# Kernel optimization log

Hardware: AMD Instinct MI355X
Metric: run time of the kernel (lower is better)

The kernel has to match this reference:

```python
import jax, jax.numpy as jnp
import numpy as np

B, L, C, H = 4, 2048, 1024, 16
D = C // H
MAX_SCALE_MUL = float(np.log(100.0))
EPS = 1e-12


def setup_inputs() -> dict:
    key = jax.random.key(0)
    ks = jax.random.split(key, 7)
    return {
        "x": jax.random.normal(ks[0], (B, L, C), dtype=jnp.float32),
        "W_qkv": jax.random.normal(ks[1], (3 * C, C), dtype=jnp.float32) * (C ** -0.5),
        "q_bias": jax.random.normal(ks[2], (C,), dtype=jnp.float32) * 0.02,
        "v_bias": jax.random.normal(ks[3], (C,), dtype=jnp.float32) * 0.02,
        "scale_mul_log": jnp.full((1, H, 1, 1), np.log(4.0), dtype=jnp.float32),
        "W_proj": jax.random.normal(ks[4], (C, C), dtype=jnp.float32) * (C ** -0.5),
        "b_proj": jax.random.normal(ks[5], (C,), dtype=jnp.float32) * 0.02,
    }


def reference(x, W_qkv, q_bias, v_bias, scale_mul_log, W_proj, b_proj):
    Bb, Ll, Cc = x.shape
    # fused QKV projection with bias = cat(q_bias, zeros, v_bias)
    bias = jnp.concatenate([q_bias, jnp.zeros_like(q_bias), v_bias])
    qkv = (x @ W_qkv.T + bias).reshape(Bb, Ll, 3, H, D)
    q, k, v = (jnp.transpose(qkv[:, :, i], (0, 2, 1, 3)) for i in range(3))  # [B,H,L,D]
    # L2-norm attention: normalize q,k; learned per-head scale on q (clamped)
    scale_mul = jnp.exp(jnp.minimum(scale_mul_log, MAX_SCALE_MUL))  # [1,H,1,1]
    q = q / jnp.maximum(jnp.linalg.norm(q, axis=-1, keepdims=True), EPS) * scale_mul
    k = k / jnp.maximum(jnp.linalg.norm(k, axis=-1, keepdims=True), EPS)
    # SDPA with scale=1 (attn_l2_norm path), no mask, no dropout (eval)
    scores = jnp.einsum("bhqd,bhkd->bhqk", q, k)
    attn = jax.nn.softmax(scores, axis=-1)
    out = jnp.einsum("bhqk,bhkd->bhqd", attn, v)
    out = jnp.transpose(out, (0, 2, 1, 3)).reshape(Bb, Ll, Cc)
    return out @ W_proj.T + b_proj
```

## Files before the change

kernel.cpp:

```cpp
#include <hip/hip_runtime.h>
#include <hip/hip_bf16.h>


typedef __attribute__((ext_vector_type(8))) short bf16x8;
typedef __attribute__((ext_vector_type(16))) float f32x16;

#define MAXLOG 4.60517018598809f
#define LOG2E  1.4426950408889634f

__device__ __forceinline__ float bf2f(unsigned short u) {
    union { unsigned int i; float f; } v; v.i = ((unsigned int)u) << 16; return v.f;
}
__device__ __forceinline__ unsigned short f2bf(float f) {
    union { float f; unsigned int i; } v; v.f = f;
    unsigned int x = v.i;
    return (unsigned short)((x + 0x7FFFu + ((x >> 16) & 1u)) >> 16);
}
__device__ __forceinline__ unsigned fbits(float f) {
    union { float f; unsigned u; } v; v.f = f; return v.u;
}
__device__ __forceinline__ bf16x8 pack8(const float* __restrict__ p) {
    float4 a = *(const float4*)p;
    float4 b = *(const float4*)(p + 4);
    bf16x8 r;
    r[0] = (short)f2bf(a.x); r[1] = (short)f2bf(a.y);
    r[2] = (short)f2bf(a.z); r[3] = (short)f2bf(a.w);
    r[4] = (short)f2bf(b.x); r[5] = (short)f2bf(b.y);
    r[6] = (short)f2bf(b.z); r[7] = (short)f2bf(b.w);
    return r;
}
__device__ __forceinline__ void gload_lds16(const void* g, void* l) {
    __builtin_amdgcn_global_load_lds((const __attribute__((address_space(1))) void*)g,
                                     (__attribute__((address_space(3))) void*)l, 16, 0, 0);
}

__global__ __launch_bounds__(256) void k_prep(
    const float* __restrict__ x, const float* __restrict__ Wqkv,
    const float* __restrict__ Wp, const float* __restrict__ qbia,
    const float* __restrict__ vbia,
    unsigned short* __restrict__ xb, unsigned short* __restrict__ Wqkvb,
    unsigned short* __restrict__ Wpb, float* __restrict__ bias3)
{
    int i = blockIdx.x * 256 + threadIdx.x;
    if (i < 1048576) {
        *(bf16x8*)&xb[(long)i * 8] = pack8(&x[(long)i * 8]);
    } else if (i < 1441792) {
        int j = i - 1048576;
        *(bf16x8*)&Wqkvb[(long)j * 8] = pack8(&Wqkv[(long)j * 8]);
    } else if (i < 1572864) {
        int j = i - 1441792;
        *(bf16x8*)&Wpb[(long)j * 8] = pack8(&Wp[(long)j * 8]);
    } else if (i < 1573248) {
        int j = (i - 1572864) * 8;
        for (int u = 0; u < 8; ++u) {
            int n = j + u;
            float v = 0.0f;
            if (n < 1024) v = qbia[n];
            else if (n >= 2048) v = vbia[n - 2048];
            bias3[n] = v;
        }
    }
}

template<bool OUT_F32>
__global__ __launch_bounds__(256) void k_gemm_lds(
    const unsigned short* __restrict__ A, const unsigned short* __restrict__ Bh,
    const float* __restrict__ bias, void* __restrict__ Cp, int N, int K)
{
    __shared__ unsigned short As[128 * 32];
    __shared__ unsigned short Bs[128 * 32];
    const int t = threadIdx.x, wave = t >> 6, lane = t & 63;
    const int m32 = lane & 31, half = lane >> 5;
    const int bm = blockIdx.x * 128, bn = blockIdx.y * 128;
    const int wr = (wave >> 1) * 64, wc = (wave & 1) * 64;
    f32x16 acc[2][2] = {};

    const int srow = lane >> 2;
    const int scol = (lane & 3) * 8;
    const int c0 = wave * 2, c1 = wave * 2 + 1;
    const long ga0 = (long)(bm + c0 * 16 + srow) * K + scol;
    const long ga1 = (long)(bm + c1 * 16 + srow) * K + scol;
    const long gb0 = (long)(bn + c0 * 16 + srow) * K + scol;
    const long gb1 = (long)(bn + c1 * 16 + srow) * K + scol;

    for (int kt = 0; kt < K; kt += 32) {
        __syncthreads();
        gload_lds16(&A[ga0 + kt], &As[c0 * 512]);
        gload_lds16(&A[ga1 + kt], &As[c1 * 512]);
        gload_lds16(&Bh[gb0 + kt], &Bs[c0 * 512]);
        gload_lds16(&Bh[gb1 + kt], &Bs[c1 * 512]);
        __syncthreads();
        bf16x8 af[2][2], bfr[2][2];
        for (int mt = 0; mt < 2; ++mt)
            for (int f = 0; f < 2; ++f)
                af[mt][f] = *(const bf16x8*)&As[(wr + mt * 32 + m32) * 32 + f * 16 + half * 8];
        for (int nt = 0; nt < 2; ++nt)
            for (int f = 0; f < 2; ++f)
                bfr[nt][f] = *(const bf16x8*)&Bs[(wc + nt * 32 + m32) * 32 + f * 16 + half * 8];
        for (int f = 0; f < 2; ++f)
            for (int mt = 0; mt < 2; ++mt)
                for (int nt = 0; nt < 2; ++nt)
                    acc[mt][nt] = __builtin_amdgcn_mfma_f32_32x32x16_bf16(
                        af[mt][f], bfr[nt][f], acc[mt][nt], 0, 0, 0);
    }
    for (int mt = 0; mt < 2; ++mt)
        for (int nt = 0; nt < 2; ++nt) {
            int gn = bn + wc + nt * 32 + m32;
            float bv = bias[gn];
            for (int r = 0; r < 16; ++r) {
                int gm = bm + wr + mt * 32 + (r & 3) + 8 * (r >> 2) + 4 * half;
                float val = acc[mt][nt][r] + bv;
                if (OUT_F32) ((float*)Cp)[(long)gm * N + gn] = val;
                else ((unsigned short*)Cp)[(long)gm * N + gn] = f2bf(val);
            }
        }
}

__global__ __launch_bounds__(256) void k_prep_kv(
    const unsigned short* __restrict__ qkv, unsigned short* __restrict__ kb,
    unsigned short* __restrict__ vT)
{
    __shared__ unsigned short Vsh[64 * 72];
    const int t = threadIdx.x;
    const int bh = blockIdx.y, l0 = blockIdx.x * 64;
    const int h = bh & 15, b = bh >> 4;
    const int ll = t >> 2, c16 = (t & 3) * 16;
    const long rowbase = (long)(b * 2048 + l0 + ll) * 3072;

    {
        bf16x8 k0 = *(const bf16x8*)&qkv[rowbase + 1024 + h * 64 + c16];
        bf16x8 k1 = *(const bf16x8*)&qkv[rowbase + 1024 + h * 64 + c16 + 8];
        float e[16]; float ss = 0.f;
        for (int j = 0; j < 8; ++j) { e[j]     = bf2f((unsigned short)k0[j]); ss += e[j] * e[j]; }
        for (int j = 0; j < 8; ++j) { e[8 + j] = bf2f((unsigned short)k1[j]); ss += e[8 + j] * e[8 + j]; }
        ss += __shfl_xor(ss, 1, 64);
        ss += __shfl_xor(ss, 2, 64);
        float rs = 1.0f / fmaxf(sqrtf(ss), 1e-12f);
        bf16x8 o0, o1;
        for (int j = 0; j < 8; ++j) o0[j] = (short)f2bf(e[j] * rs);
        for (int j = 0; j < 8; ++j) o1[j] = (short)f2bf(e[8 + j] * rs);
        long dst = ((long)bh * 2048 + l0 + ll) * 64 + c16;
        *(bf16x8*)&kb[dst]     = o0;
        *(bf16x8*)&kb[dst + 8] = o1;
    }
    *(bf16x8*)&Vsh[ll * 72 + c16]     = *(const bf16x8*)&qkv[rowbase + 2048 + h * 64 + c16];
    *(bf16x8*)&Vsh[ll * 72 + c16 + 8] = *(const bf16x8*)&qkv[rowbase + 2048 + h * 64 + c16 + 8];
    __syncthreads();
    const int d = t >> 2, ls = (t & 3) * 16;
    unsigned short tmp[16];
    for (int j = 0; j < 16; ++j) tmp[j] = Vsh[(ls + j) * 72 + d];
    long dst = (long)(bh * 64 + d) * 2048 + l0 + ls;
    *(bf16x8*)&vT[dst]     = *(bf16x8*)&tmp[0];
    *(bf16x8*)&vT[dst + 8] = *(bf16x8*)&tmp[8];
}

__global__ __launch_bounds__(256, 4) void k_attn32(
    const unsigned short* __restrict__ qkv, const unsigned short* __restrict__ kb,
    const unsigned short* __restrict__ vT, const float* __restrict__ sml,
    unsigned short* __restrict__ attn)
{
    __shared__ unsigned short Ks[2][64 * 72];
    __shared__ unsigned short Vs[2][64 * 72];
    const int t = threadIdx.x, wave = t >> 6, lane = t & 63;
    const int m32 = lane & 31, half = lane >> 5;
    const int bh = blockIdx.y, h = bh & 15, b = bh >> 4;
    const int q0 = blockIdx.x * 128 + wave * 32;
    const float scale = __expf(fminf(sml[h], MAXLOG));
    const float c2 = scale * LOG2E;

    const int qd = m32 >> 2, lo = qd & 3;
    const int prow = ((((lo == 1) || (lo == 2)) ? (qd ^ 3) : qd) << 2) | (m32 & 3);

    bf16x8 aq[4];
    {
        long base = (long)(b * 2048 + q0 + m32) * 3072 + h * 64;
        float e[32]; float ss = 0.f;
        for (int f = 0; f < 4; ++f) {
            aq[f] = *(const bf16x8*)&qkv[base + f * 16 + half * 8];
            for (int j = 0; j < 8; ++j) { float x = bf2f((unsigned short)aq[f][j]); e[f * 8 + j] = x; ss += x * x; }
        }
        ss += __shfl_xor(ss, 32, 64);
        float rs = (scale * LOG2E) / fmaxf(sqrtf(ss), 1e-12f);
        for (int f = 0; f < 4; ++f)
            for (int j = 0; j < 8; ++j) aq[f][j] = (short)f2bf(e[f * 8 + j] * rs);
    }

    f32x16 o0 = {}, o1 = {}, lacc = {};
    bf16x8 ones; for (int i = 0; i < 8; ++i) ones[i] = (short)0x3F80;
    const int sr = t >> 2, sc = (t & 3) * 16;
    const long kbase = (long)bh * 2048 * 64;
    const long vbase = (long)bh * 64 * 2048;

#define LOADT(kt) \
    kpA = *(const bf16x8*)&kb[kbase + (long)((kt) + sr) * 64 + sc];      \
    kpB = *(const bf16x8*)&kb[kbase + (long)((kt) + sr) * 64 + sc + 8];  \
    vpA = *(const bf16x8*)&vT[vbase + (long)sr * 2048 + (kt) + sc];      \
    vpB = *(const bf16x8*)&vT[vbase + (long)sr * 2048 + (kt) + sc + 8];

#define STORET(buf) \
    *(bf16x8*)&Ks[buf][sr * 72 + sc]     = kpA;  \
    *(bf16x8*)&Ks[buf][sr * 72 + sc + 8] = kpB;  \
    *(bf16x8*)&Vs[buf][sr * 72 + sc]     = vpA;  \
    *(bf16x8*)&Vs[buf][sr * 72 + sc + 8] = vpB;

#define ATTN_STEP(KS, VS, SUB) \
    for (int ktile = 0; ktile < 2; ++ktile) {                                              \
        const unsigned short* krow = &KS[(ktile * 32 + prow) * 72 + half * 8];             \
        f32x16 s = {};                                                                     \
        s = __builtin_amdgcn_mfma_f32_32x32x16_bf16(*(const bf16x8*)&krow[0],  aq[0], s, 0, 0, 0); \
        s = __builtin_amdgcn_mfma_f32_32x32x16_bf16(*(const bf16x8*)&krow[16], aq[1], s, 0, 0, 0); \
        s = __builtin_amdgcn_mfma_f32_32x32x16_bf16(*(const bf16x8*)&krow[32], aq[2], s, 0, 0, 0); \
        s = __builtin_amdgcn_mfma_f32_32x32x16_bf16(*(const bf16x8*)&krow[48], aq[3], s, 0, 0, 0); \
        unsigned pu[16];                                                                   \
        for (int j = 0; j < 16; ++j)                                                       \
            pu[j] = fbits(__builtin_amdgcn_exp2f(s[j] - (SUB)));                           \
        uint4 a0u, a1u;                                                                    \
        a0u.x = __builtin_amdgcn_perm(pu[1],  pu[0],  0x07060302u);                        \
        a0u.y = __builtin_amdgcn_perm(pu[3],  pu[2],  0x07060302u);                        \
        a0u.z = __builtin_amdgcn_perm(pu[5],  pu[4],  0x07060302u);                        \
        a0u.w = __builtin_amdgcn_perm(pu[7],  pu[6],  0x07060302u);                        \
        a1u.x = __builtin_amdgcn_perm(pu[9],  pu[8],  0x07060302u);                        \
        a1u.y = __builtin_amdgcn_perm(pu[11], pu[10], 0x07060302u);                        \
        a1u.z = __builtin_amdgcn_perm(pu[13], pu[12], 0x07060302u);                        \
        a1u.w = __builtin_amdgcn_perm(pu[15], pu[14], 0x07060302u);                        \
        bf16x8 ap0, ap1;                                                                   \
        __builtin_memcpy(&ap0, &a0u, 16); __builtin_memcpy(&ap1, &a1u, 16);                \
        for (int c = 0; c < 2; ++c) {                                                      \
            bf16x8 apc = c ? ap1 : ap0;                                                    \
            bf16x8 bv0 = *(const bf16x8*)&VS[m32 * 72        + ktile * 32 + c * 16 + half * 8]; \
            bf16x8 bv1 = *(const bf16x8*)&VS[(32 + m32) * 72 + ktile * 32 + c * 16 + half * 8]; \
            o0   = __builtin_amdgcn_mfma_f32_32x32x16_bf16(apc, bv0, o0, 0, 0, 0);         \
            o1   = __builtin_amdgcn_mfma_f32_32x32x16_bf16(apc, bv1, o1, 0, 0, 0);         \
            lacc = __builtin_amdgcn_mfma_f32_32x32x16_bf16(apc, ones, lacc, 0, 0, 0);      \
        }                                                                                  \
    }

#define KLOOP(SUB) \
    for (int kt = 0; kt < 2048; kt += 128) {                 \
        LOADT(kt + 64)                                       \
        ATTN_STEP(Ks[0], Vs[0], SUB)                         \
        STORET(1)                                            \
        __syncthreads();                                     \
        const bool more = (kt + 128) < 2048;                 \
        if (more) { LOADT(kt + 128) }                        \
        ATTN_STEP(Ks[1], Vs[1], SUB)                         \
        if (more) {                                          \
            STORET(0)                                        \
            __syncthreads();                                 \
        }                                                    \
    }

    bf16x8 kpA, kpB, vpA, vpB;
    LOADT(0)
    STORET(0)
    __syncthreads();

    if (c2 < 30.0f) {
        KLOOP(0.0f)
    } else {
        KLOOP(c2)
    }
#undef LOADT
#undef STORET
#undef ATTN_STEP
#undef KLOOP

    for (int r = 0; r < 16; ++r) {
        int m = (r & 3) + 8 * (r >> 2) + 4 * half;
        float inv = 1.0f / lacc[r];
        long dst = (long)(b * 2048 + q0 + m) * 1024 + h * 64;
        attn[dst + m32]      = f2bf(o0[r] * inv);
        attn[dst + 32 + m32] = f2bf(o1[r] * inv);
    }
}

extern "C" void kernel_launch(void* const* d_in, const int* in_sizes, int n_in,
                              void* d_out, int out_size, void* d_ws, size_t ws_size,
                              hipStream_t stream) {
    const float* x    = (const float*)d_in[0];
    const float* Wqkv = (const float*)d_in[1];
    const float* qbia = (const float*)d_in[2];
    const float* vbia = (const float*)d_in[3];
    const float* sml  = (const float*)d_in[4];
    const float* Wp   = (const float*)d_in[5];
    const float* bp   = (const float*)d_in[6];

    char* ws = (char*)d_ws;
    unsigned short* qkv   = (unsigned short*)ws;
    unsigned short* kbuf  = (unsigned short*)(ws + 50331648);
    unsigned short* Wqkvb = kbuf;
    unsigned short* vT    = (unsigned short*)(ws + 67108864);
    unsigned short* xb    = vT;
    unsigned short* attnb = (unsigned short*)(ws + 83886080);
    float*          bias3 = (float*)(ws + 100663296);
    unsigned short* Wpb   = (unsigned short*)(ws + 100679680);
    float*          out   = (float*)d_out;

    hipLaunchKernelGGL(k_prep, dim3(6146), dim3(256), 0, stream,
                       x, Wqkv, Wp, qbia, vbia, xb, Wqkvb, Wpb, bias3);
    hipLaunchKernelGGL((k_gemm_lds<false>), dim3(64, 24), dim3(256), 0, stream,
                       xb, Wqkvb, bias3, (void*)qkv, 3072, 1024);
    hipLaunchKernelGGL(k_prep_kv, dim3(32, 64), dim3(256), 0, stream, qkv, kbuf, vT);
    hipLaunchKernelGGL(k_attn32, dim3(16, 64), dim3(256), 0, stream, qkv, kbuf, vT, sml, attnb);
    hipLaunchKernelGGL((k_gemm_lds<true>), dim3(64, 8), dim3(256), 0, stream,
                       attnb, Wpb, bp, (void*)out, 1024, 1024);
}
```

Measured before the change: 297.8 us.

## Read K/V directly from global memory in attention, drop LDS staging and ones-MFMA

The attention kernel no longer stages K and V tiles through double-buffered shared memory with barriers. Each wave now loads its MFMA operands straight from global memory and relies on L2/cache reuse. The softmax row sum moves from an extra MFMA against a ones vector to a scalar accumulation of the bf16-truncated probabilities, reduced with shuffles. A 1D grid with XCD-aware remapping groups the blocks of one head onto the same XCD for cache locality. This trades the LDS traffic and syncs for uncoalesced, redundant global loads across the four waves of each block.

```diff
diff --git a/kernel.cpp b/kernel.cpp
--- a/kernel.cpp
+++ b/kernel.cpp
@@ -18,6 +18,9 @@
 }
 __device__ __forceinline__ unsigned fbits(float f) {
     union { float f; unsigned u; } v; v.f = f; return v.u;
+}
+__device__ __forceinline__ float uasf(unsigned u) {
+    union { unsigned u; float f; } v; v.u = u; return v.f;
 }
 __device__ __forceinline__ bf16x8 pack8(const float* __restrict__ p) {
     float4 a = *(const float4*)p;
@@ -159,12 +162,13 @@
     const unsigned short* __restrict__ vT, const float* __restrict__ sml,
     unsigned short* __restrict__ attn)
 {
-    __shared__ unsigned short Ks[2][64 * 72];
-    __shared__ unsigned short Vs[2][64 * 72];
     const int t = threadIdx.x, wave = t >> 6, lane = t & 63;
     const int m32 = lane & 31, half = lane >> 5;
-    const int bh = blockIdx.y, h = bh & 15, b = bh >> 4;
-    const int q0 = blockIdx.x * 128 + wave * 32;
+    const int wg = blockIdx.x;
+    const int logical = (wg & 7) * 128 + (wg >> 3);
+    const int bh = logical >> 4, qblk = logical & 15;
+    const int h = bh & 15, b = bh >> 4;
+    const int q0 = qblk * 128 + wave * 32;
     const float scale = __expf(fminf(sml[h], MAXLOG));
     const float c2 = scale * LOG2E;
 
@@ -185,35 +189,29 @@
             for (int j = 0; j < 8; ++j) aq[f][j] = (short)f2bf(e[f * 8 + j] * rs);
     }
 
-    f32x16 o0 = {}, o1 = {}, lacc = {};
-    bf16x8 ones; for (int i = 0; i < 8; ++i) ones[i] = (short)0x3F80;
-    const int sr = t >> 2, sc = (t & 3) * 16;
+    f32x16 o0 = {}, o1 = {};
+    float rowacc = 0.f;
     const long kbase = (long)bh * 2048 * 64;
     const long vbase = (long)bh * 64 * 2048;
-
-#define LOADT(kt) \
-    kpA = *(const bf16x8*)&kb[kbase + (long)((kt) + sr) * 64 + sc];      \
-    kpB = *(const bf16x8*)&kb[kbase + (long)((kt) + sr) * 64 + sc + 8];  \
-    vpA = *(const bf16x8*)&vT[vbase + (long)sr * 2048 + (kt) + sc];      \
-    vpB = *(const bf16x8*)&vT[vbase + (long)sr * 2048 + (kt) + sc + 8];
-
-#define STORET(buf) \
-    *(bf16x8*)&Ks[buf][sr * 72 + sc]     = kpA;  \
-    *(bf16x8*)&Ks[buf][sr * 72 + sc + 8] = kpB;  \
-    *(bf16x8*)&Vs[buf][sr * 72 + sc]     = vpA;  \
-    *(bf16x8*)&Vs[buf][sr * 72 + sc + 8] = vpB;
-
-#define ATTN_STEP(KS, VS, SUB) \
+    const unsigned short* kp  = &kb[kbase + (long)prow * 64 + half * 8];
+    const unsigned short* vp0 = &vT[vbase + (long)m32 * 2048 + half * 8];
+    const unsigned short* vp1 = vp0 + 32 * 2048;
+
+#define ATTN_STEP(kt, SUB) \
     for (int ktile = 0; ktile < 2; ++ktile) {                                              \
-        const unsigned short* krow = &KS[(ktile * 32 + prow) * 72 + half * 8];             \
+        const unsigned short* krow = kp + (long)((kt) + ktile * 32) * 64;                  \
         f32x16 s = {};                                                                     \
         s = __builtin_amdgcn_mfma_f32_32x32x16_bf16(*(const bf16x8*)&krow[0],  aq[0], s, 0, 0, 0); \
         s = __builtin_amdgcn_mfma_f32_32x32x16_bf16(*(const bf16x8*)&krow[16], aq[1], s, 0, 0, 0); \
         s = __builtin_amdgcn_mfma_f32_32x32x16_bf16(*(const bf16x8*)&krow[32], aq[2], s, 0, 0, 0); \
         s = __builtin_amdgcn_mfma_f32_32x32x16_bf16(*(const bf16x8*)&krow[48], aq[3], s, 0, 0, 0); \
-        unsigned pu[16];                                                                   \
-        for (int j = 0; j < 16; ++j)                                                       \
-            pu[j] = fbits(__builtin_amdgcn_exp2f(s[j] - (SUB)));                           \
+        unsigned pu[16]; float psum = 0.f;                                                 \
+        for (int j = 0; j < 16; ++j) {                                                     \
+            unsigned pb = fbits(__builtin_amdgcn_exp2f(s[j] - (SUB)));                     \
+            pu[j] = pb;                                                                    \
+            psum += uasf(pb & 0xFFFF0000u);                   \
+        }                                                                                  \
+        rowacc += psum;                                                                    \
         uint4 a0u, a1u;                                                                    \
         a0u.x = __builtin_amdgcn_perm(pu[1],  pu[0],  0x07060302u);                        \
         a0u.y = __builtin_amdgcn_perm(pu[3],  pu[2],  0x07060302u);                        \
@@ -227,47 +225,26 @@
         __builtin_memcpy(&ap0, &a0u, 16); __builtin_memcpy(&ap1, &a1u, 16);                \
         for (int c = 0; c < 2; ++c) {                                                      \
             bf16x8 apc = c ? ap1 : ap0;                                                    \
-            bf16x8 bv0 = *(const bf16x8*)&VS[m32 * 72        + ktile * 32 + c * 16 + half * 8]; \
-            bf16x8 bv1 = *(const bf16x8*)&VS[(32 + m32) * 72 + ktile * 32 + c * 16 + half * 8]; \
-            o0   = __builtin_amdgcn_mfma_f32_32x32x16_bf16(apc, bv0, o0, 0, 0, 0);         \
-            o1   = __builtin_amdgcn_mfma_f32_32x32x16_bf16(apc, bv1, o1, 0, 0, 0);         \
-            lacc = __builtin_amdgcn_mfma_f32_32x32x16_bf16(apc, ones, lacc, 0, 0, 0);      \
+            bf16x8 bv0 = *(const bf16x8*)(vp0 + (kt) + ktile * 32 + c * 16);               \
+            bf16x8 bv1 = *(const bf16x8*)(vp1 + (kt) + ktile * 32 + c * 16);               \
+            o0 = __builtin_amdgcn_mfma_f32_32x32x16_bf16(apc, bv0, o0, 0, 0, 0);           \
+            o1 = __builtin_amdgcn_mfma_f32_32x32x16_bf16(apc, bv1, o1, 0, 0, 0);           \
         }                                                                                  \
     }
 
-#define KLOOP(SUB) \
-    for (int kt = 0; kt < 2048; kt += 128) {                 \
-        LOADT(kt + 64)                                       \
-        ATTN_STEP(Ks[0], Vs[0], SUB)                         \
-        STORET(1)                                            \
-        __syncthreads();                                     \
-        const bool more = (kt + 128) < 2048;                 \
-        if (more) { LOADT(kt + 128) }                        \
-        ATTN_STEP(Ks[1], Vs[1], SUB)                         \
-        if (more) {                                          \
-            STORET(0)                                        \
-            __syncthreads();                                 \
-        }                                                    \
-    }
-
-    bf16x8 kpA, kpB, vpA, vpB;
-    LOADT(0)
-    STORET(0)
-    __syncthreads();
-
     if (c2 < 30.0f) {
-        KLOOP(0.0f)
+#pragma unroll 2
+        for (int kt = 0; kt < 2048; kt += 64) { ATTN_STEP(kt, 0.0f) }
     } else {
-        KLOOP(c2)
-    }
-#undef LOADT
-#undef STORET
+#pragma unroll 2
+        for (int kt = 0; kt < 2048; kt += 64) { ATTN_STEP(kt, c2) }
+    }
 #undef ATTN_STEP
-#undef KLOOP
-
+
+    float rtot = rowacc + __shfl_xor(rowacc, 32, 64);
     for (int r = 0; r < 16; ++r) {
         int m = (r & 3) + 8 * (r >> 2) + 4 * half;
-        float inv = 1.0f / lacc[r];
+        float inv = 1.0f / __shfl(rtot, m, 64);
         long dst = (long)(b * 2048 + q0 + m) * 1024 + h * 64;
         attn[dst + m32]      = f2bf(o0[r] * inv);
         attn[dst + 32 + m32] = f2bf(o1[r] * inv);
@@ -301,7 +278,7 @@
     hipLaunchKernelGGL((k_gemm_lds<false>), dim3(64, 24), dim3(256), 0, stream,
                        xb, Wqkvb, bias3, (void*)qkv, 3072, 1024);
     hipLaunchKernelGGL(k_prep_kv, dim3(32, 64), dim3(256), 0, stream, qkv, kbuf, vT);
-    hipLaunchKernelGGL(k_attn32, dim3(16, 64), dim3(256), 0, stream, qkv, kbuf, vT, sml, attnb);
+    hipLaunchKernelGGL(k_attn32, dim3(1024), dim3(256), 0, stream, qkv, kbuf, vT, sml, attnb);
     hipLaunchKernelGGL((k_gemm_lds<true>), dim3(64, 8), dim3(256), 0, stream,
                        attnb, Wpb, bp, (void*)out, 1024, 1024);
 }
```

Result: slower. 439.1 us (+47.4%).

## Compute softmax row sums in VALU and swizzle attention grid across XCDs

Applied to the files above, without the earlier changes.

The softmax denominator used to be built with an extra MFMA against a ones vector on every P·V step. It is now summed from the fp32 exponentials in registers, combined across the two half-waves with a shuffle, and broadcast per output row at the end. This cuts the matrix-core work in the inner loop by a third, at the cost of some extra VALU adds and shuffles. The grid is also flattened to 1D and remapped so that consecutive blocks, which land on different XCDs, end up with each XCD handling contiguous query blocks of the same heads. That should improve L2 reuse of K and V. The normalizer now sums unrounded fp32 values while P is fed to the MFMA in bf16, a small numeric difference.

```diff
diff --git a/kernel.cpp b/kernel.cpp
--- a/kernel.cpp
+++ b/kernel.cpp
@@ -163,8 +163,11 @@
     __shared__ unsigned short Vs[2][64 * 72];
     const int t = threadIdx.x, wave = t >> 6, lane = t & 63;
     const int m32 = lane & 31, half = lane >> 5;
-    const int bh = blockIdx.y, h = bh & 15, b = bh >> 4;
-    const int q0 = blockIdx.x * 128 + wave * 32;
+    const int wg = blockIdx.x;
+    const int logical = (wg & 7) * 128 + (wg >> 3);
+    const int bh = logical >> 4, qblk = logical & 15;
+    const int h = bh & 15, b = bh >> 4;
+    const int q0 = qblk * 128 + wave * 32;
     const float scale = __expf(fminf(sml[h], MAXLOG));
     const float c2 = scale * LOG2E;
 
@@ -185,8 +188,8 @@
             for (int j = 0; j < 8; ++j) aq[f][j] = (short)f2bf(e[f * 8 + j] * rs);
     }
 
-    f32x16 o0 = {}, o1 = {}, lacc = {};
-    bf16x8 ones; for (int i = 0; i < 8; ++i) ones[i] = (short)0x3F80;
+    f32x16 o0 = {}, o1 = {};
+    float rowacc = 0.f;
     const int sr = t >> 2, sc = (t & 3) * 16;
     const long kbase = (long)bh * 2048 * 64;
     const long vbase = (long)bh * 64 * 2048;
@@ -212,8 +215,17 @@
         s = __builtin_amdgcn_mfma_f32_32x32x16_bf16(*(const bf16x8*)&krow[32], aq[2], s, 0, 0, 0); \
         s = __builtin_amdgcn_mfma_f32_32x32x16_bf16(*(const bf16x8*)&krow[48], aq[3], s, 0, 0, 0); \
         unsigned pu[16];                                                                   \
-        for (int j = 0; j < 16; ++j)                                                       \
-            pu[j] = fbits(__builtin_amdgcn_exp2f(s[j] - (SUB)));                           \
+        float p0 = 0.f, p1 = 0.f, p2 = 0.f, p3 = 0.f;                                      \
+        for (int j = 0; j < 4; ++j) {                                                      \
+            float e0 = __builtin_amdgcn_exp2f(s[j]      - (SUB));                          \
+            float e1 = __builtin_amdgcn_exp2f(s[4 + j]  - (SUB));                          \
+            float e2 = __builtin_amdgcn_exp2f(s[8 + j]  - (SUB));                          \
+            float e3 = __builtin_amdgcn_exp2f(s[12 + j] - (SUB));                          \
+            pu[j] = fbits(e0); pu[4 + j] = fbits(e1);                                      \
+            pu[8 + j] = fbits(e2); pu[12 + j] = fbits(e3);                                 \
+            p0 += e0; p1 += e1; p2 += e2; p3 += e3;                                        \
+        }                                                                                  \
+        rowacc += (p0 + p1) + (p2 + p3);                                                   \
         uint4 a0u, a1u;                                                                    \
         a0u.x = __builtin_amdgcn_perm(pu[1],  pu[0],  0x07060302u);                        \
         a0u.y = __builtin_amdgcn_perm(pu[3],  pu[2],  0x07060302u);                        \
@@ -229,9 +241,8 @@
             bf16x8 apc = c ? ap1 : ap0;                                                    \
             bf16x8 bv0 = *(const bf16x8*)&VS[m32 * 72        + ktile * 32 + c * 16 + half * 8]; \
             bf16x8 bv1 = *(const bf16x8*)&VS[(32 + m32) * 72 + ktile * 32 + c * 16 + half * 8]; \
-            o0   = __builtin_amdgcn_mfma_f32_32x32x16_bf16(apc, bv0, o0, 0, 0, 0);         \
-            o1   = __builtin_amdgcn_mfma_f32_32x32x16_bf16(apc, bv1, o1, 0, 0, 0);         \
-            lacc = __builtin_amdgcn_mfma_f32_32x32x16_bf16(apc, ones, lacc, 0, 0, 0);      \
+            o0 = __builtin_amdgcn_mfma_f32_32x32x16_bf16(apc, bv0, o0, 0, 0, 0);           \
+            o1 = __builtin_amdgcn_mfma_f32_32x32x16_bf16(apc, bv1, o1, 0, 0, 0);           \
         }                                                                                  \
     }
 
@@ -265,9 +276,10 @@
 #undef ATTN_STEP
 #undef KLOOP
 
+    float rtot = rowacc + __shfl_xor(rowacc, 32, 64);
     for (int r = 0; r < 16; ++r) {
         int m = (r & 3) + 8 * (r >> 2) + 4 * half;
-        float inv = 1.0f / lacc[r];
+        float inv = 1.0f / __shfl(rtot, m, 64);
         long dst = (long)(b * 2048 + q0 + m) * 1024 + h * 64;
         attn[dst + m32]      = f2bf(o0[r] * inv);
         attn[dst + 32 + m32] = f2bf(o1[r] * inv);
@@ -301,7 +313,7 @@
     hipLaunchKernelGGL((k_gemm_lds<false>), dim3(64, 24), dim3(256), 0, stream,
                        xb, Wqkvb, bias3, (void*)qkv, 3072, 1024);
     hipLaunchKernelGGL(k_prep_kv, dim3(32, 64), dim3(256), 0, stream, qkv, kbuf, vT);
-    hipLaunchKernelGGL(k_attn32, dim3(16, 64), dim3(256), 0, stream, qkv, kbuf, vT, sml, attnb);
+    hipLaunchKernelGGL(k_attn32, dim3(1024), dim3(256), 0, stream, qkv, kbuf, vT, sml, attnb);
     hipLaunchKernelGGL((k_gemm_lds<true>), dim3(64, 8), dim3(256), 0, stream,
                        attnb, Wpb, bp, (void*)out, 1024, 1024);
 }
```

After: 496.7 us. +66.8%, slower.
